# Kernel optimization log

Hardware: AMD Instinct MI355X
Metric: run time of the kernel (lower is better)

Reference implementation:

```python
import jax, jax.numpy as jnp
import numpy as np

# Faithful JAX port of torchvision rotate(img, -angle, BILINEAR) applied to every
# (image, angle) pair, matching torchvision's align_corners=False grid_sample math:
# for output pixel (yo, xo), with a = radians(angle) (sign of the module's -angle
# already folded in), centered coords X = xo-(W-1)/2, Y = yo-(H-1)/2:
#   src_x = cos(a)*X - sin(a)*Y + (W-1)/2
#   src_y = sin(a)*X + cos(a)*Y + (H-1)/2
# then bilinear sample with zero padding outside the image.

def rotate_batch(image_batch, angles):
    n, c, H, W = image_batch.shape  # c == 1 (required by original output assignment)
    img = image_batch[:, 0]         # (n, H, W)
    a = jnp.deg2rad(angles)         # (k,)
    cx = (W - 1) * 0.5
    cy = (H - 1) * 0.5
    X = (jnp.arange(W, dtype=image_batch.dtype) - cx)[None, None, :]  # (1,1,W)
    Y = (jnp.arange(H, dtype=image_batch.dtype) - cy)[None, :, None]  # (1,H,1)
    ca = jnp.cos(a)[:, None, None]  # (k,1,1)
    sa = jnp.sin(a)[:, None, None]
    sx = ca * X - sa * Y + cx       # (k,H,W) source x in pixel coords
    sy = sa * X + ca * Y + cy       # (k,H,W)

    x0f = jnp.floor(sx); y0f = jnp.floor(sy)
    wx = sx - x0f; wy = sy - y0f    # bilinear fractional weights
    x0 = x0f.astype(jnp.int32); y0 = y0f.astype(jnp.int32)
    x1 = x0 + 1; y1 = y0 + 1

    def gather(yi, xi):
        # zero-padding grid_sample: out-of-bounds corners contribute 0
        valid = (yi >= 0) & (yi < H) & (xi >= 0) & (xi < W)      # (k,H,W)
        yc = jnp.clip(yi, 0, H - 1)
        xc = jnp.clip(xi, 0, W - 1)
        vals = img[:, yc, xc]                                     # (n,k,H,W)
        return jnp.where(valid[None], vals, jnp.zeros((), image_batch.dtype))

    out = (gather(y0, x0) * ((1 - wy) * (1 - wx))[None]
         + gather(y0, x1) * ((1 - wy) * wx)[None]
         + gather(y1, x0) * (wy * (1 - wx))[None]
         + gather(y1, x1) * (wy * wx)[None])
    return out  # (n, k, H, W)


def setup_inputs() -> dict:
    key = jax.random.key(0)
    k_img, k_ang = jax.random.split(key)
    image_batch = jax.random.normal(k_img, (32, 1, 512, 512), dtype=jnp.float32)
    angles = jax.random.uniform(k_ang, (8,), dtype=jnp.float32) * 360.0  # degrees
    return {"image_batch": image_batch, "angles": angles}


def reference(image_batch, angles):
    return rotate_batch(image_batch, angles)
```

## Files before the change

### kernel.cpp

```cpp
#include <hip/hip_runtime.h>
#include <math.h>
#include <stdint.h>

#define N_IMG 32
#define N_ANG 8
#define H_ 512
#define W_ 512

#define TX 64
#define TY 32
#define LP 84
#define MAXCH 25
#define LWORDS (MAXCH * 256)
#define OP 68

typedef float f32x4 __attribute__((ext_vector_type(4)));

__global__ __launch_bounds__(256, 3) void rotate_tile_kernel(
    const float* __restrict__ img,
    const float* __restrict__ angles,
    float* __restrict__ out)
{
    __shared__ float tile[2 * LWORDS];

    const int bz   = blockIdx.z;
    const int k    = bz >> 1;
    const int n0   = (bz & 1) * (N_IMG / 2);
    const int tx0  = blockIdx.x * TX;
    const int ty0  = blockIdx.y * TY;
    const int tid  = threadIdx.x;
    const int wid  = tid >> 6;
    const int lane = tid & 63;

    const float rad = angles[k] * 0.017453292519943295f;
    float sa, ca;
    sincosf(rad, &sa, &ca);
    const float cx = (W_ - 1) * 0.5f;
    const float cy = (H_ - 1) * 0.5f;

    float minsx = 1e30f, maxsx = -1e30f, minsy = 1e30f, maxsy = -1e30f;
#pragma unroll
    for (int cyi = 0; cyi < 2; ++cyi) {
#pragma unroll
        for (int cxi = 0; cxi < 2; ++cxi) {
            const float xr = (float)(tx0 + cxi * (TX - 1)) - cx;
            const float yr = (float)(ty0 + cyi * (TY - 1)) - cy;
            const float sx = ca * xr - sa * yr + cx;
            const float sy = sa * xr + ca * yr + cy;
            minsx = fminf(minsx, sx); maxsx = fmaxf(maxsx, sx);
            minsy = fminf(minsy, sy); maxsy = fmaxf(maxsy, sy);
        }
    }
    const int bx0 = min(max((int)floorf(minsx) - 1, 0), W_ - 1);
    const int by0 = min(max((int)floorf(minsy) - 1, 0), H_ - 1);
    const int bx0m = (bx0 & ~3) - 4;
    const int by0m = by0 - 1;
    const int rowsS  = min((int)floorf(maxsy) + 2 - by0m, 76);
    const int nchunk = min((rowsS * LP + 255) >> 8, MAXCH);

    int goff[7];
    int nst = 0;
    for (int s = wid; s < nchunk; s += 4) {
        const int f   = s * 256 + lane * 4;
        const int row = f / LP;
        const int col = f - row * LP;
        const int grow = min(max(by0m + row, 0), H_ - 1);
        const int gcol = min(max(bx0m + col, 0), W_ - 4);
        goff[nst++] = grow * W_ + gcol;
    }

    const bool modeA = fabsf(ca) >= fabsf(sa);
    const int pxg = modeA ? (tid & 15) : (tid >> 4);
    const int py0 = modeA ? (tid >> 4) : (tid & 15);
    const int px  = pxg * 4;

    int   ob[2][4];
    float w00[2][4], w01[2][4], w10[2][4], w11[2][4];
#pragma unroll
    for (int p = 0; p < 2; ++p) {
        const int   yy = ty0 + py0 + p * 16;
        const float yr = (float)yy - cy;
#pragma unroll
        for (int j = 0; j < 4; ++j) {
            const int   xx = tx0 + px + j;
            const float xr = (float)xx - cx;
            const float sxs = ca * xr - sa * yr + cx;
            const float sys = sa * xr + ca * yr + cy;
            const float x0f = floorf(sxs), y0f = floorf(sys);
            const float wx = sxs - x0f, wy = sys - y0f;
            const int x0 = (int)x0f, y0 = (int)y0f;
            const bool vx0 = ((unsigned)x0       < (unsigned)W_);
            const bool vx1 = ((unsigned)(x0 + 1) < (unsigned)W_);
            const bool vy0 = ((unsigned)y0       < (unsigned)H_);
            const bool vy1 = ((unsigned)(y0 + 1) < (unsigned)H_);
            const int lx = min(max(x0 - bx0m, 0), 82);
            const int ly = min(max(y0 - by0m, 0), rowsS - 2);
            ob[p][j] = ly * LP + lx;
            const float omwx = 1.0f - wx, omwy = 1.0f - wy;
            w00[p][j] = omwy * omwx * (float)(vy0 && vx0);
            w01[p][j] = omwy * wx   * (float)(vy0 && vx1);
            w10[p][j] = wy   * omwx * (float)(vy1 && vx0);
            w11[p][j] = wy   * wx   * (float)(vy1 && vx1);
        }
    }

    auto stage_img = [&](int n, int b) {
        const float* __restrict__ ib = img + (size_t)n * (H_ * W_);
        float* dst0 = &tile[b * LWORDS];
        for (int i = 0; i < nst; ++i) {
            __builtin_amdgcn_global_load_lds(
                (const __attribute__((address_space(1))) void*)(ib + goff[i]),
                (__attribute__((address_space(3))) void*)(dst0 + (wid + i * 4) * 256),
                16, 0, 0);
        }
    };

    stage_img(n0, 0);
    asm volatile("s_waitcnt vmcnt(0)" ::: "memory");
    __builtin_amdgcn_s_barrier();

    int cur = 0;
    for (int idx = 0; idx < N_IMG / 2; ++idx) {
        const int n = n0 + idx;
        const bool more = (idx + 1 < N_IMG / 2);
        if (more) {
            stage_img(n + 1, cur ^ 1);
            __builtin_amdgcn_sched_barrier(0);
        }

        const float* __restrict__ tb = &tile[cur * LWORDS];
        float* __restrict__ outn =
            out + ((size_t)(n * N_ANG + k) * H_ + ty0) * W_ + tx0;

        float v[2][4];
#pragma unroll
        for (int p = 0; p < 2; ++p) {
#pragma unroll
            for (int j = 0; j < 4; ++j) {
                const float* __restrict__ b0 = &tb[ob[p][j]];
                v[p][j] = w00[p][j] * b0[0]
                        + w01[p][j] * b0[1]
                        + w10[p][j] * b0[LP]
                        + w11[p][j] * b0[LP + 1];
            }
        }

        if (modeA) {
#pragma unroll
            for (int p = 0; p < 2; ++p) {
                f32x4 vv = { v[p][0], v[p][1], v[p][2], v[p][3] };
                __builtin_nontemporal_store(
                    vv, (f32x4*)(outn + (py0 + p * 16) * W_ + px));
            }
        } else {
            __builtin_amdgcn_s_barrier();
            float* __restrict__ os = (float*)&tile[cur * LWORDS];
#pragma unroll
            for (int p = 0; p < 2; ++p) {
                f32x4 vv = { v[p][0], v[p][1], v[p][2], v[p][3] };
                *(f32x4*)(os + (py0 + p * 16) * OP + px) = vv;
            }
            asm volatile("s_waitcnt lgkmcnt(0)" ::: "memory");
            __builtin_amdgcn_sched_barrier(0);
            __builtin_amdgcn_s_barrier();
            const int rx = (tid & 15) * 4;
            const int ry = tid >> 4;
#pragma unroll
            for (int p = 0; p < 2; ++p) {
                f32x4 t = *(f32x4*)(os + (ry + p * 16) * OP + rx);
                __builtin_nontemporal_store(
                    t, (f32x4*)(outn + (ry + p * 16) * W_ + rx));
            }
        }

        if (more) {
            asm volatile("s_waitcnt vmcnt(2)" ::: "memory");
            __builtin_amdgcn_s_barrier();
            cur ^= 1;
        }
    }
}

extern "C" void kernel_launch(void* const* d_in, const int* in_sizes, int n_in,
                              void* d_out, int out_size, void* d_ws, size_t ws_size,
                              hipStream_t stream) {
    const float* img    = (const float*)d_in[0];
    const float* angles = (const float*)d_in[1];
    float* out          = (float*)d_out;

    dim3 block(256, 1, 1);
    dim3 grid(W_ / TX, H_ / TY, N_ANG * 2);
    rotate_tile_kernel<<<grid, block, 0, stream>>>(img, angles, out);
}
```

Baseline: 332.0 us.

## Replace LDS-staged source tiles with direct paired global gathers

Removes the double-buffered LDS staging of each rotated source footprint (global_load_lds plus barriers) and instead gathers the bilinear corners straight from global memory as two 8-byte loads per output pixel, relying on L1/L2 caching. Edge handling is moved into the weights by clamping x0 and swapping weights when x0 is -1 or W-1. LDS use shrinks to a small transpose buffer, so occupancy is raised to 5 blocks per CU. The risk is more scattered global/cache traffic and less explicit latency hiding compared with the prefetch pipeline.

```diff
diff --git a/kernel.cpp b/kernel.cpp
--- a/kernel.cpp
+++ b/kernel.cpp
@@ -6,22 +6,21 @@
 #define N_ANG 8
 #define H_ 512
 #define W_ 512
+#define HW (H_ * W_)
 
 #define TX 64
 #define TY 32
-#define LP 84
-#define MAXCH 25
-#define LWORDS (MAXCH * 256)
 #define OP 68
 
 typedef float f32x4 __attribute__((ext_vector_type(4)));
+typedef float f32x2 __attribute__((ext_vector_type(2)));
 
-__global__ __launch_bounds__(256, 3) void rotate_tile_kernel(
+__global__ __launch_bounds__(256, 5) void rotate_tile_kernel(
     const float* __restrict__ img,
     const float* __restrict__ angles,
     float* __restrict__ out)
 {
-    __shared__ float tile[2 * LWORDS];
+    __shared__ float osb[TY * OP];
 
     const int bz   = blockIdx.z;
     const int k    = bz >> 1;
@@ -29,8 +28,6 @@
     const int tx0  = blockIdx.x * TX;
     const int ty0  = blockIdx.y * TY;
     const int tid  = threadIdx.x;
-    const int wid  = tid >> 6;
-    const int lane = tid & 63;
 
     const float rad = angles[k] * 0.017453292519943295f;
     float sa, ca;
@@ -38,43 +35,12 @@
     const float cx = (W_ - 1) * 0.5f;
     const float cy = (H_ - 1) * 0.5f;
 
-    float minsx = 1e30f, maxsx = -1e30f, minsy = 1e30f, maxsy = -1e30f;
-#pragma unroll
-    for (int cyi = 0; cyi < 2; ++cyi) {
-#pragma unroll
-        for (int cxi = 0; cxi < 2; ++cxi) {
-            const float xr = (float)(tx0 + cxi * (TX - 1)) - cx;
-            const float yr = (float)(ty0 + cyi * (TY - 1)) - cy;
-            const float sx = ca * xr - sa * yr + cx;
-            const float sy = sa * xr + ca * yr + cy;
-            minsx = fminf(minsx, sx); maxsx = fmaxf(maxsx, sx);
-            minsy = fminf(minsy, sy); maxsy = fmaxf(maxsy, sy);
-        }
-    }
-    const int bx0 = min(max((int)floorf(minsx) - 1, 0), W_ - 1);
-    const int by0 = min(max((int)floorf(minsy) - 1, 0), H_ - 1);
-    const int bx0m = (bx0 & ~3) - 4;
-    const int by0m = by0 - 1;
-    const int rowsS  = min((int)floorf(maxsy) + 2 - by0m, 76);
-    const int nchunk = min((rowsS * LP + 255) >> 8, MAXCH);
-
-    int goff[7];
-    int nst = 0;
-    for (int s = wid; s < nchunk; s += 4) {
-        const int f   = s * 256 + lane * 4;
-        const int row = f / LP;
-        const int col = f - row * LP;
-        const int grow = min(max(by0m + row, 0), H_ - 1);
-        const int gcol = min(max(bx0m + col, 0), W_ - 4);
-        goff[nst++] = grow * W_ + gcol;
-    }
-
     const bool modeA = fabsf(ca) >= fabsf(sa);
     const int pxg = modeA ? (tid & 15) : (tid >> 4);
     const int py0 = modeA ? (tid >> 4) : (tid & 15);
     const int px  = pxg * 4;
 
-    int   ob[2][4];
+    int   o0[2][4], o1[2][4];
     float w00[2][4], w01[2][4], w10[2][4], w11[2][4];
 #pragma unroll
     for (int p = 0; p < 2; ++p) {
@@ -93,42 +59,25 @@
             const bool vx1 = ((unsigned)(x0 + 1) < (unsigned)W_);
             const bool vy0 = ((unsigned)y0       < (unsigned)H_);
             const bool vy1 = ((unsigned)(y0 + 1) < (unsigned)H_);
-            const int lx = min(max(x0 - bx0m, 0), 82);
-            const int ly = min(max(y0 - by0m, 0), rowsS - 2);
-            ob[p][j] = ly * LP + lx;
+            const int xb  = min(max(x0, 0), W_ - 2);
+            const int yc0 = min(max(y0, 0), H_ - 1);
+            const int yc1 = min(max(y0 + 1, 0), H_ - 1);
+            o0[p][j] = yc0 * W_ + xb;
+            o1[p][j] = yc1 * W_ + xb;
             const float omwx = 1.0f - wx, omwy = 1.0f - wy;
-            w00[p][j] = omwy * omwx * (float)(vy0 && vx0);
-            w01[p][j] = omwy * wx   * (float)(vy0 && vx1);
-            w10[p][j] = wy   * omwx * (float)(vy1 && vx0);
-            w11[p][j] = wy   * wx   * (float)(vy1 && vx1);
+            float a = omwy * omwx * (float)(vy0 && vx0);
+            float b = omwy * wx   * (float)(vy0 && vx1);
+            float c = wy   * omwx * (float)(vy1 && vx0);
+            float d = wy   * wx   * (float)(vy1 && vx1);
+            if (x0 == -1)      { a = b; b = 0.0f; c = d; d = 0.0f; }
+            else if (x0 == W_ - 1) { b = a; a = 0.0f; d = c; c = 0.0f; }
+            w00[p][j] = a; w01[p][j] = b; w10[p][j] = c; w11[p][j] = d;
         }
     }
 
-    auto stage_img = [&](int n, int b) {
-        const float* __restrict__ ib = img + (size_t)n * (H_ * W_);
-        float* dst0 = &tile[b * LWORDS];
-        for (int i = 0; i < nst; ++i) {
-            __builtin_amdgcn_global_load_lds(
-                (const __attribute__((address_space(1))) void*)(ib + goff[i]),
-                (__attribute__((address_space(3))) void*)(dst0 + (wid + i * 4) * 256),
-                16, 0, 0);
-        }
-    };
-
-    stage_img(n0, 0);
-    asm volatile("s_waitcnt vmcnt(0)" ::: "memory");
-    __builtin_amdgcn_s_barrier();
-
-    int cur = 0;
     for (int idx = 0; idx < N_IMG / 2; ++idx) {
         const int n = n0 + idx;
-        const bool more = (idx + 1 < N_IMG / 2);
-        if (more) {
-            stage_img(n + 1, cur ^ 1);
-            __builtin_amdgcn_sched_barrier(0);
-        }
-
-        const float* __restrict__ tb = &tile[cur * LWORDS];
+        const float* __restrict__ ibc = img + (size_t)n * HW;
         float* __restrict__ outn =
             out + ((size_t)(n * N_ANG + k) * H_ + ty0) * W_ + tx0;
 
@@ -137,11 +86,10 @@
         for (int p = 0; p < 2; ++p) {
 #pragma unroll
             for (int j = 0; j < 4; ++j) {
-                const float* __restrict__ b0 = &tb[ob[p][j]];
-                v[p][j] = w00[p][j] * b0[0]
-                        + w01[p][j] * b0[1]
-                        + w10[p][j] * b0[LP]
-                        + w11[p][j] * b0[LP + 1];
+                const f32x2 L0 = *(const f32x2*)(ibc + o0[p][j]);
+                const f32x2 L1 = *(const f32x2*)(ibc + o1[p][j]);
+                v[p][j] = w00[p][j] * L0.x + w01[p][j] * L0.y
+                        + w10[p][j] * L1.x + w11[p][j] * L1.y;
             }
         }
 
@@ -153,12 +101,10 @@
                     vv, (f32x4*)(outn + (py0 + p * 16) * W_ + px));
             }
         } else {
-            __builtin_amdgcn_s_barrier();
-            float* __restrict__ os = (float*)&tile[cur * LWORDS];
 #pragma unroll
             for (int p = 0; p < 2; ++p) {
                 f32x4 vv = { v[p][0], v[p][1], v[p][2], v[p][3] };
-                *(f32x4*)(os + (py0 + p * 16) * OP + px) = vv;
+                *(f32x4*)(osb + (py0 + p * 16) * OP + px) = vv;
             }
             asm volatile("s_waitcnt lgkmcnt(0)" ::: "memory");
             __builtin_amdgcn_sched_barrier(0);
@@ -167,16 +113,13 @@
             const int ry = tid >> 4;
 #pragma unroll
             for (int p = 0; p < 2; ++p) {
-                f32x4 t = *(f32x4*)(os + (ry + p * 16) * OP + rx);
+                f32x4 t = *(f32x4*)(osb + (ry + p * 16) * OP + rx);
                 __builtin_nontemporal_store(
                     t, (f32x4*)(outn + (ry + p * 16) * W_ + rx));
             }
-        }
-
-        if (more) {
-            asm volatile("s_waitcnt vmcnt(2)" ::: "memory");
+            asm volatile("s_waitcnt lgkmcnt(0)" ::: "memory");
+            __builtin_amdgcn_sched_barrier(0);
             __builtin_amdgcn_s_barrier();
-            cur ^= 1;
         }
     }
 }
```

After: 442.4 us. +33.2%, slower.
